# Performance work log

Measured on AMD Instinct MI355X. Metric: run time of the kernel, lower is better.

Reference implementation:

```python
import jax, jax.numpy as jnp
import numpy as np

BOS, PAD, EOS, UNK = 0, 1, 2, 3  # fairseq dictionary special-token ids
CHAR_VOCAB = 5000
DIM = 512
LATENT = 10000


def setup_inputs() -> dict:
    key = jax.random.key(0)
    k1, k2, k3 = jax.random.split(key, 3)
    # char-ngram ids per token: [B, T, max_char_len]
    x = jax.random.randint(k1, (8, 1024, 20), 0, CHAR_VOCAB, dtype=jnp.int64 if jax.config.jax_enable_x64 else jnp.int32)
    # char ngram embedding table (also serves as preset_emb for special tokens)
    char_table = jax.random.normal(k2, (CHAR_VOCAB, DIM), dtype=jnp.float32) * 0.05
    # fixed latent codebook, init std = latent**-0.5 as in the module
    latent_mat = jax.random.normal(k3, (LATENT, DIM), dtype=jnp.float32) * (LATENT ** -0.5)
    return {"x": x, "char_table": char_table, "latent_mat": latent_mat}


def reference(x, char_table, latent_mat):
    # --- CharacterNgramEmbedder: gather + sum-pool over char ngrams (pad masked) ---
    emb = char_table[x]                                   # [B, T, C, D]
    valid = (x != PAD)[..., None].astype(emb.dtype)       # pad ngrams contribute 0
    ngram_weight = jnp.sum(emb * valid, axis=2)           # [B, T, D]
    lang_emb = jnp.tanh(ngram_weight)

    # --- latent codebook attention: QK^T -> softmax -> V over fixed codebook ---
    latent_scores = jnp.einsum('btd,ld->btl', lang_emb, latent_mat)   # [B, T, L]
    latent_dist = jax.nn.softmax(latent_scores, axis=-1)
    latent_emb = jnp.einsum('btl,ld->btd', latent_dist, latent_mat)   # [B, T, D]
    sde_emb = lang_emb + latent_emb

    # --- preset_emb overwrite for special tokens (masked scatter) ---
    first = x[:, :, 0]                                    # [B, T]
    for tok in (PAD, BOS, EOS, UNK):
        sde_emb = jnp.where((first == tok)[..., None], char_table[tok], sde_emb)
    return sde_emb
```

## Files before the change

kernel.cpp:

```cpp
#include <hip/hip_runtime.h>

#define BT    8192
#define DIM   512
#define NLAT  10000
#define LPAD2 10240
#define NG    20
#define CV    5000

typedef short bf16x8 __attribute__((ext_vector_type(8)));
typedef float f32x4  __attribute__((ext_vector_type(4)));
typedef unsigned short u16;
typedef u16 u16x8 __attribute__((ext_vector_type(8)));
typedef u16 u16x4 __attribute__((ext_vector_type(4)));

static __device__ __forceinline__ u16 f2bf(float f) {
    union { float f; unsigned u; } v; v.f = f;
    unsigned r = v.u + 0x7FFF + ((v.u >> 16) & 1);
    return (u16)(r >> 16);
}
static __device__ __forceinline__ float bf2f(u16 b) {
    union { unsigned u; float f; } v; v.u = ((unsigned)b) << 16; return v.f;
}

static __device__ __forceinline__ void gload16(const void* g, void* l) {
    __builtin_amdgcn_global_load_lds(
        (const __attribute__((address_space(1))) unsigned int*)g,
        (__attribute__((address_space(3))) unsigned int*)l,
        16, 0, 0);
}

__global__ __launch_bounds__(256) void ct2bf_kernel(
        const float* __restrict__ ct, u16* __restrict__ ctb) {
    const long base = ((long)blockIdx.x * 256 + threadIdx.x) * 8;
    float4 a = *(const float4*)(ct + base);
    float4 b = *(const float4*)(ct + base + 4);
    u16x8 v = { f2bf(a.x), f2bf(a.y), f2bf(a.z), f2bf(a.w),
                f2bf(b.x), f2bf(b.y), f2bf(b.z), f2bf(b.w) };
    *(u16x8*)(ctb + base) = v;
}

__global__ __launch_bounds__(256) void lang_kernel(
        const int* __restrict__ x, const u16* __restrict__ ctb,
        float* __restrict__ lang, u16* __restrict__ qb) {
    const int wv  = threadIdx.x >> 6;
    const int tl  = threadIdx.x & 63;
    const int tok0 = blockIdx.x * 8 + wv * 2;
    const int* xr0 = x + tok0 * NG;
    const int* xr1 = xr0 + NG;
    float s0[8], s1[8];
    #pragma unroll
    for (int i = 0; i < 8; ++i) { s0[i] = 0.f; s1[i] = 0.f; }
    #pragma unroll
    for (int j = 0; j < NG; ++j) {
        int c0 = xr0[j], c1 = xr1[j];
        if (c0 != 1) {
            u16x8 v = *(const u16x8*)(ctb + (long)c0 * DIM + tl * 8);
            #pragma unroll
            for (int i = 0; i < 8; ++i) s0[i] += bf2f(v[i]);
        }
        if (c1 != 1) {
            u16x8 v = *(const u16x8*)(ctb + (long)c1 * DIM + tl * 8);
            #pragma unroll
            for (int i = 0; i < 8; ++i) s1[i] += bf2f(v[i]);
        }
    }
    #pragma unroll
    for (int p = 0; p < 2; ++p) {
        float* s = p ? s1 : s0;
        const long tok = tok0 + p;
        float4 lo, hi;
        lo.x = tanhf(s[0]); lo.y = tanhf(s[1]); lo.z = tanhf(s[2]); lo.w = tanhf(s[3]);
        hi.x = tanhf(s[4]); hi.y = tanhf(s[5]); hi.z = tanhf(s[6]); hi.w = tanhf(s[7]);
        *(float4*)(lang + tok * DIM + tl * 8)     = lo;
        *(float4*)(lang + tok * DIM + tl * 8 + 4) = hi;
        u16x8 o = { f2bf(lo.x), f2bf(lo.y), f2bf(lo.z), f2bf(lo.w),
                    f2bf(hi.x), f2bf(hi.y), f2bf(hi.z), f2bf(hi.w) };
        *(u16x8*)(qb + tok * DIM + tl * 8) = o;
    }
}

__global__ __launch_bounds__(256) void conv_kernel(
        const float* __restrict__ lm, u16* __restrict__ kvg, u16* __restrict__ latT) {
    __shared__ u16 tile[64][514];
    const int lb = blockIdx.x * 64;
    const int t  = threadIdx.x;

    #pragma unroll 4
    for (int i = 0; i < 16; ++i) {
        int ch  = t + i * 256;
        int r   = ch >> 6;
        int c8  = ch & 63;
        int row = lb + r;
        u16x8 v = {0,0,0,0,0,0,0,0};
        if (row < NLAT) {
            const float* src = lm + (long)row * DIM + c8 * 8;
            float4 a = *(const float4*)src;
            float4 b = *(const float4*)(src + 4);
            v[0]=f2bf(a.x); v[1]=f2bf(a.y); v[2]=f2bf(a.z); v[3]=f2bf(a.w);
            v[4]=f2bf(b.x); v[5]=f2bf(b.y); v[6]=f2bf(b.z); v[7]=f2bf(b.w);
        }
        *(u16x8*)(kvg + (long)row * DIM + c8 * 8) = v;
        #pragma unroll
        for (int j = 0; j < 8; ++j) tile[r][c8 * 8 + j] = v[j];
    }
    __syncthreads();
    #pragma unroll 4
    for (int i = 0; i < 16; ++i) {
        int ch = t + i * 256;
        int d  = ch >> 3;
        int c8 = ch & 7;
        u16x8 v;
        #pragma unroll
        for (int j = 0; j < 8; ++j) v[j] = tile[c8 * 8 + j][d];
        *(u16x8*)(latT + (long)d * LPAD2 + lb + c8 * 8) = v;
    }
}

#define G1_STAGE(buf, kt) {                                                    \
    const int k0_ = (kt) * 32;                                                 \
    {                                                                          \
        int ch_ = t;                                                           \
        int row_ = ch_ >> 2, c2_ = ch_ & 3;                                    \
        int sc_ = (c2_ ^ ((row_ >> 1) & 3)) * 8;                               \
        gload16(Q + (m0 + row_) * (long)DIM + k0_ + sc_, &lds[buf][ch_ * 8]);  \
        ch_ = t + 512; row_ = ch_ >> 2; c2_ = ch_ & 3;                         \
        sc_ = (c2_ ^ ((row_ >> 1) & 3)) * 8;                                   \
        gload16(Q + (m0 + row_) * (long)DIM + k0_ + sc_, &lds[buf][ch_ * 8]);  \
        row_ = t >> 2; c2_ = t & 3;                                            \
        sc_ = (c2_ ^ ((row_ >> 1) & 3)) * 8;                                   \
        gload16(Bgp + (long)row_ * DIM + k0_ + sc_, &lds[buf][8192 + t * 8]);  \
    }                                                                          \
}

#define G1_COMPUTE(buf) {                                                      \
    bf16x8 af_[4], bf_[4];                                                     \
    _Pragma("unroll")                                                          \
    for (int mf_ = 0; mf_ < 4; ++mf_) {                                        \
        const int rA_ = wm * 64 + mf_ * 16 + lr;                               \
        const int ck_ = g ^ ((rA_ >> 1) & 3);                                  \
        af_[mf_] = *(const bf16x8*)&lds[buf][rA_ * 32 + ck_ * 8];              \
    }                                                                          \
    _Pragma("unroll")                                                          \
    for (int nf_ = 0; nf_ < 4; ++nf_) {                                        \
        const int rB_ = wn * 64 + nf_ * 16 + lr;                               \
        const int ck_ = g ^ ((rB_ >> 1) & 3);                                  \
        bf_[nf_] = *(const bf16x8*)&lds[buf][8192 + rB_ * 32 + ck_ * 8];       \
    }                                                                          \
    __builtin_amdgcn_s_setprio(1);                                             \
    _Pragma("unroll")                                                          \
    for (int mf_ = 0; mf_ < 4; ++mf_)                                          \
        _Pragma("unroll")                                                      \
        for (int nf_ = 0; nf_ < 4; ++nf_)                                      \
            acc[mf_][nf_] = __builtin_amdgcn_mfma_f32_16x16x32_bf16(           \
                af_[mf_], bf_[nf_], acc[mf_][nf_], 0, 0, 0);                   \
    __builtin_amdgcn_s_setprio(0);                                             \
}

#define G1_STEP(kt, vmn) {                                                     \
    asm volatile("s_waitcnt vmcnt(" #vmn ")" ::: "memory");                    \
    __builtin_amdgcn_s_barrier();                                              \
    G1_COMPUTE((kt) % 3);                                                      \
    __builtin_amdgcn_s_barrier();                                              \
}

__global__ __launch_bounds__(512, 4) void gemm1_kernel(
        const u16* __restrict__ Q, const u16* __restrict__ L,
        u16* __restrict__ P, float* __restrict__ rowsum,
        int n0_global, int npanels, int pstride) {
    __shared__ u16 lds[3][12288];

    const int nwg = 32 * npanels;
    const int cpx = nwg >> 3;
    const int bid = blockIdx.x;
    const int wg  = (bid & 7) * cpx + (bid >> 3);
    int mb, nb;
    if (npanels == 80) {
        const int st = wg / 80, lt = wg % 80;
        const int lmb = lt & 7, lnb = lt >> 3;
        const int smb = st & 3, snb = st >> 2;
        mb = smb * 8 + lmb;
        nb = snb * 10 + lnb;
    } else {
        mb = wg & 31;
        nb = wg >> 5;
    }
    const long m0    = (long)mb * 256;
    const int  ncol0 = n0_global + nb * 128;

    const u16* Bgp = L + (long)ncol0 * DIM;

    const int t = threadIdx.x, lane = t & 63, w = t >> 6;
    const int wm = w >> 1, wn = w & 1;
    const int g = lane >> 4, lr = lane & 15;

    f32x4 acc[4][4];
    #pragma unroll
    for (int m = 0; m < 4; ++m)
        #pragma unroll
        for (int n = 0; n < 4; ++n) acc[m][n] = f32x4{0.f,0.f,0.f,0.f};

    G1_STAGE(0, 0);
    G1_STAGE(1, 1);
    G1_STAGE(2, 2);

    #pragma unroll 1
    for (int kt = 0; kt < 13; ++kt) {
        asm volatile("s_waitcnt vmcnt(6)" ::: "memory");
        __builtin_amdgcn_s_barrier();
        G1_COMPUTE(kt % 3);
        __builtin_amdgcn_s_barrier();
        G1_STAGE(kt % 3, kt + 3);
    }
    G1_STEP(13, 6);
    G1_STEP(14, 3);
    asm volatile("s_waitcnt vmcnt(0)" ::: "memory");
    __builtin_amdgcn_s_barrier();
    G1_COMPUTE(15 % 3);
    __syncthreads();

    u16* lds16 = &lds[0][0];
    #pragma unroll
    for (int mf = 0; mf < 4; ++mf)
        #pragma unroll
        for (int nf = 0; nf < 4; ++nf) {
            const int col = ncol0 + wn * 64 + nf * 16 + lr;
            const bool ok = (col < NLAT);
            const int lcol = wn * 64 + nf * 16 + lr;
            #pragma unroll
            for (int r = 0; r < 4; ++r) {
                float p = ok ? __expf(acc[mf][nf][r]) : 0.f;
                acc[mf][nf][r] = p;
                const int row = wm * 64 + mf * 16 + g * 4 + r;
                lds16[row * 128 + (lcol ^ ((row & 15) << 3))] = f2bf(p);
            }
        }

    #pragma unroll
    for (int mf = 0; mf < 4; ++mf) {
        float sv[4] = {0.f, 0.f, 0.f, 0.f};
        #pragma unroll
        for (int nf = 0; nf < 4; ++nf)
            #pragma unroll
            for (int r = 0; r < 4; ++r) sv[r] += acc[mf][nf][r];
        #pragma unroll
        for (int r = 0; r < 4; ++r) {
            float s = sv[r];
            s += __shfl_xor(s, 1); s += __shfl_xor(s, 2);
            s += __shfl_xor(s, 4); s += __shfl_xor(s, 8);
            if (lr == 0)
                atomicAdd(&rowsum[m0 + wm * 64 + mf * 16 + g * 4 + r], s);
        }
    }

    __syncthreads();
    const int pbase = ncol0 - n0_global;
    #pragma unroll
    for (int it = 0; it < 8; ++it) {
        const int flat = t + it * 512;
        const int row = flat >> 4, ck = flat & 15;
        u16x8 v = *(const u16x8*)&lds16[row * 128 + ((ck ^ (row & 15)) * 8)];
        *(u16x8*)(P + (m0 + row) * (long)pstride + pbase + ck * 8) = v;
    }
}

#define G_COMPUTE(buf) {                                                       \
    _Pragma("unroll")                                                          \
    for (int kc_ = 0; kc_ < 2; ++kc_) {                                        \
        const int xs_ = ((kc_ * 4 + g) ^ (lr & 7)) * 8;                        \
        bf16x8 af_[2], bf_[4];                                                 \
        _Pragma("unroll")                                                      \
        for (int mf_ = 0; mf_ < 2; ++mf_)                                      \
            af_[mf_] = *(const bf16x8*)&lds[buf][(wm * 32 + mf_ * 16 + lr) * 64 + xs_]; \
        _Pragma("unroll")                                                      \
        for (int nf_ = 0; nf_ < 4; ++nf_)                                      \
            bf_[nf_] = *(const bf16x8*)&lds[buf][8192 + (wn * 64 + nf_ * 16 + lr) * 64 + xs_]; \
        __builtin_amdgcn_s_setprio(1);                                         \
        _Pragma("unroll")                                                      \
        for (int mf_ = 0; mf_ < 2; ++mf_)                                      \
            _Pragma("unroll")                                                  \
            for (int nf_ = 0; nf_ < 4; ++nf_)                                  \
                acc[mf_][nf_] = __builtin_amdgcn_mfma_f32_16x16x32_bf16(       \
                    af_[mf_], bf_[nf_], acc[mf_][nf_], 0, 0, 0);               \
        __builtin_amdgcn_s_setprio(0);                                         \
    }                                                                          \
}

#define G2_STAGE(buf, kt) {                                                    \
    const int kloc_ = (step_off + (kt)) * 64;                                  \
    _Pragma("unroll")                                                          \
    for (int i_ = 0; i_ < 2; ++i_) {                                           \
        int ch_ = t + i_ * 512;                                                \
        int row_ = ch_ >> 3;                                                   \
        int sc_ = ((ch_ & 7) ^ (row_ & 7)) * 8;                                \
        gload16(P + (m0 + row_) * (long)pstride + kloc_ + sc_, &lds[buf][ch_ * 8]); \
        gload16(LT + (long)(nbase + row_) * LPAD2 + n0_global + kloc_ + sc_,   \
                &lds[buf][8192 + ch_ * 8]);                                    \
    }                                                                          \
}

__global__ __launch_bounds__(512, 4) void gemm2_kernel(
        const u16* __restrict__ P, const u16* __restrict__ LT,
        float* __restrict__ out, float* __restrict__ part0,
        int pstride, int kcols, int n0_global, int splitk, int accum) {
    __shared__ u16 lds[2][16384];

    const int nwg = 64 * 4 * splitk;
    const int cpx = nwg >> 3;
    const int bid = blockIdx.x;
    const int wg  = (bid & 7) * cpx + (bid >> 3);
    const int mb  = wg & 63;
    const int rest = wg >> 6;
    const int nb  = rest / splitk;
    const int s   = rest % splitk;

    const long m0    = (long)mb * 128;
    const int  nbase = nb * 128;

    const int nsteps = kcols / 64;
    const int q = nsteps / splitk, rr = nsteps % splitk;
    const int psteps   = q + (s < rr ? 1 : 0);
    const int step_off = s * q + (s < rr ? s : rr);

    const int t = threadIdx.x, lane = t & 63, w = t >> 6;
    const int wm = w >> 1, wn = w & 1;
    const int g = lane >> 4, lr = lane & 15;

    float* buf = (s == 0) ? out : part0;

    f32x4 acc[2][4];
    #pragma unroll
    for (int m = 0; m < 2; ++m)
        #pragma unroll
        for (int n = 0; n < 4; ++n) acc[m][n] = f32x4{0.f,0.f,0.f,0.f};

    G2_STAGE(0, 0);
    if (psteps > 1) G2_STAGE(1, 1);

    #pragma unroll 1
    for (int kt = 0; kt < psteps - 1; ++kt) {
        asm volatile("s_waitcnt vmcnt(4)" ::: "memory");
        __builtin_amdgcn_s_barrier();
        G_COMPUTE(kt & 1);
        __builtin_amdgcn_s_barrier();
        if (kt + 2 < psteps) G2_STAGE(kt & 1, kt + 2);
    }
    asm volatile("s_waitcnt vmcnt(0)" ::: "memory");
    __builtin_amdgcn_s_barrier();
    G_COMPUTE((psteps - 1) & 1);

    #pragma unroll
    for (int mf = 0; mf < 2; ++mf)
        #pragma unroll
        for (int nf = 0; nf < 4; ++nf) {
            const int col = nbase + wn * 64 + nf * 16 + lr;
            #pragma unroll
            for (int r = 0; r < 4; ++r) {
                const long row = m0 + wm * 32 + mf * 16 + g * 4 + r;
                float v = acc[mf][nf][r];
                if (accum) v += buf[row * DIM + col];
                buf[row * DIM + col] = v;
            }
        }
}

__global__ __launch_bounds__(256) void final_kernel(
        float* __restrict__ out, const float* __restrict__ part0,
        const float* __restrict__ lang, const float* __restrict__ rowsum,
        const int* __restrict__ x, const float* __restrict__ ct, int nparts) {
    const int tok   = blockIdx.x;
    const float inv = 1.f / rowsum[tok];
    const int first = x[tok * NG];
    #pragma unroll
    for (int i = 0; i < 2; ++i) {
        const int col = threadIdx.x + i * 256;
        float v = out[(long)tok * DIM + col];
        if (nparts > 1) v += part0[(long)tok * DIM + col];
        v = v * inv + lang[(long)tok * DIM + col];
        if (first < 4) v = ct[first * DIM + col];
        out[(long)tok * DIM + col] = v;
    }
}

extern "C" void kernel_launch(void* const* d_in, const int* in_sizes, int n_in,
                              void* d_out, int out_size, void* d_ws, size_t ws_size,
                              hipStream_t stream) {
    const int*   x  = (const int*)d_in[0];
    const float* ct = (const float*)d_in[1];
    const float* lm = (const float*)d_in[2];
    float* out = (float*)d_out;

    char* ws = (char*)d_ws;
    size_t off = 0;
    u16*   qb   = (u16*)(ws + off);   off += (size_t)BT * DIM * 2;
    float* lang = (float*)(ws + off); off += (size_t)BT * DIM * 4;
    u16*   kvg  = (u16*)(ws + off);   off += (size_t)LPAD2 * DIM * 2;
    u16*   latT = (u16*)(ws + off);   off += (size_t)DIM * LPAD2 * 2;
    u16*   ctb  = (u16*)(ws + off);   off += (size_t)CV * DIM * 2;
    float* rowsum = (float*)(ws + off); off += (size_t)BT * 4;
    u16*   P    = (u16*)(ws + off);
    const size_t fixed = off;

    const int panels_total = LPAD2 / 128;
    const size_t pfull = (size_t)BT * LPAD2 * 2;
    const size_t partb = (size_t)BT * DIM * 4;

    int splitk = 1, ppc = panels_total;
    float* part0 = out;
    if (ws_size >= fixed + pfull + partb) {
        splitk = 2;
        part0 = (float*)(ws + fixed + pfull);
    } else if (ws_size >= fixed + pfull) {
        splitk = 1;
    } else {
        size_t avail = (ws_size > fixed) ? (ws_size - fixed) : 0;
        size_t p = avail / ((size_t)BT * 128 * 2);
        ppc = (int)(p < 1 ? 1 : (p > (size_t)panels_total ? (size_t)panels_total : p));
        if (ppc & 1) ppc = (ppc > 1) ? ppc - 1 : 1;
    }
    const int pstride = ppc * 128;

    hipMemsetAsync(rowsum, 0, (size_t)BT * 4, stream);
    ct2bf_kernel<<<CV * DIM / (256 * 8), 256, 0, stream>>>(ct, ctb);
    lang_kernel<<<BT / 8, 256, 0, stream>>>(x, ctb, lang, qb);
    conv_kernel<<<LPAD2 / 64, 256, 0, stream>>>(lm, kvg, latT);

    int chunk = 0;
    for (int cs = 0; cs < panels_total; cs += ppc, ++chunk) {
        const int np = (panels_total - cs < ppc) ? (panels_total - cs) : ppc;
        gemm1_kernel<<<32 * np, 512, 0, stream>>>(qb, kvg, P, rowsum,
                                                  cs * 128, np, pstride);
        gemm2_kernel<<<64 * 4 * splitk, 512, 0, stream>>>(P, latT, out, part0,
                                                          pstride, np * 128, cs * 128,
                                                          splitk, chunk > 0 ? 1 : 0);
    }
    final_kernel<<<BT, 256, 0, stream>>>(out, part0, lang, rowsum, x, ct, splitk);
}
```

Baseline: 286.2 us.

## Retile gemm2 to 256x128 tiles with triple-buffered pipeline and split-K of four

The second GEMM (P @ latT) now uses the gemm1 tile shape: 256x128 output tiles, a K step of 32 and three LDS buffers in a deeper prefetch pipeline. This replaces 128x128 tiles with a K step of 64 and double buffering. Split-K rises from 2 to 4 when workspace allows, and the final kernel sums a variable number of partial buffers. The larger tiles raise data reuse per workgroup, and the higher split-K keeps enough workgroups to fill the GPU. The cost is more partial-sum traffic, more accumulator registers, and a fixed three-stage prologue that assumes each split has at least three K steps.

After: 272.7 us. -4.7%, faster.

```diff
diff --git a/kernel.cpp b/kernel.cpp
--- a/kernel.cpp
+++ b/kernel.cpp
@@ -114,22 +114,6 @@
         for (int j = 0; j < 8; ++j) v[j] = tile[c8 * 8 + j][d];
         *(u16x8*)(latT + (long)d * LPAD2 + lb + c8 * 8) = v;
     }
-}
-
-#define G1_STAGE(buf, kt) {                                                    \
-    const int k0_ = (kt) * 32;                                                 \
-    {                                                                          \
-        int ch_ = t;                                                           \
-        int row_ = ch_ >> 2, c2_ = ch_ & 3;                                    \
-        int sc_ = (c2_ ^ ((row_ >> 1) & 3)) * 8;                               \
-        gload16(Q + (m0 + row_) * (long)DIM + k0_ + sc_, &lds[buf][ch_ * 8]);  \
-        ch_ = t + 512; row_ = ch_ >> 2; c2_ = ch_ & 3;                         \
-        sc_ = (c2_ ^ ((row_ >> 1) & 3)) * 8;                                   \
-        gload16(Q + (m0 + row_) * (long)DIM + k0_ + sc_, &lds[buf][ch_ * 8]);  \
-        row_ = t >> 2; c2_ = t & 3;                                            \
-        sc_ = (c2_ ^ ((row_ >> 1) & 3)) * 8;                                   \
-        gload16(Bgp + (long)row_ * DIM + k0_ + sc_, &lds[buf][8192 + t * 8]);  \
-    }                                                                          \
 }
 
 #define G1_COMPUTE(buf) {                                                      \
@@ -156,6 +140,22 @@
     __builtin_amdgcn_s_setprio(0);                                             \
 }
 
+#define G1_STAGE(buf, kt) {                                                    \
+    const int k0_ = (kt) * 32;                                                 \
+    {                                                                          \
+        int ch_ = t;                                                           \
+        int row_ = ch_ >> 2, c2_ = ch_ & 3;                                    \
+        int sc_ = (c2_ ^ ((row_ >> 1) & 3)) * 8;                               \
+        gload16(Q + (m0 + row_) * (long)DIM + k0_ + sc_, &lds[buf][ch_ * 8]);  \
+        ch_ = t + 512; row_ = ch_ >> 2; c2_ = ch_ & 3;                         \
+        sc_ = (c2_ ^ ((row_ >> 1) & 3)) * 8;                                   \
+        gload16(Q + (m0 + row_) * (long)DIM + k0_ + sc_, &lds[buf][ch_ * 8]);  \
+        row_ = t >> 2; c2_ = t & 3;                                            \
+        sc_ = (c2_ ^ ((row_ >> 1) & 3)) * 8;                                   \
+        gload16(Bgp + (long)row_ * DIM + k0_ + sc_, &lds[buf][8192 + t * 8]);  \
+    }                                                                          \
+}
+
 #define G1_STEP(kt, vmn) {                                                     \
     asm volatile("s_waitcnt vmcnt(" #vmn ")" ::: "memory");                    \
     __builtin_amdgcn_s_barrier();                                              \
@@ -263,99 +263,95 @@
     }
 }
 
-#define G_COMPUTE(buf) {                                                       \
-    _Pragma("unroll")                                                          \
-    for (int kc_ = 0; kc_ < 2; ++kc_) {                                        \
-        const int xs_ = ((kc_ * 4 + g) ^ (lr & 7)) * 8;                        \
-        bf16x8 af_[2], bf_[4];                                                 \
-        _Pragma("unroll")                                                      \
-        for (int mf_ = 0; mf_ < 2; ++mf_)                                      \
-            af_[mf_] = *(const bf16x8*)&lds[buf][(wm * 32 + mf_ * 16 + lr) * 64 + xs_]; \
-        _Pragma("unroll")                                                      \
-        for (int nf_ = 0; nf_ < 4; ++nf_)                                      \
-            bf_[nf_] = *(const bf16x8*)&lds[buf][8192 + (wn * 64 + nf_ * 16 + lr) * 64 + xs_]; \
-        __builtin_amdgcn_s_setprio(1);                                         \
-        _Pragma("unroll")                                                      \
-        for (int mf_ = 0; mf_ < 2; ++mf_)                                      \
-            _Pragma("unroll")                                                  \
-            for (int nf_ = 0; nf_ < 4; ++nf_)                                  \
-                acc[mf_][nf_] = __builtin_amdgcn_mfma_f32_16x16x32_bf16(       \
-                    af_[mf_], bf_[nf_], acc[mf_][nf_], 0, 0, 0);               \
-        __builtin_amdgcn_s_setprio(0);                                         \
-    }                                                                          \
-}
-
 #define G2_STAGE(buf, kt) {                                                    \
-    const int kloc_ = (step_off + (kt)) * 64;                                  \
-    _Pragma("unroll")                                                          \
-    for (int i_ = 0; i_ < 2; ++i_) {                                           \
-        int ch_ = t + i_ * 512;                                                \
-        int row_ = ch_ >> 3;                                                   \
-        int sc_ = ((ch_ & 7) ^ (row_ & 7)) * 8;                                \
+    const int kloc_ = (step_off + (kt)) * 32;                                  \
+    {                                                                          \
+        int ch_ = t;                                                           \
+        int row_ = ch_ >> 2, c2_ = ch_ & 3;                                    \
+        int sc_ = (c2_ ^ ((row_ >> 1) & 3)) * 8;                               \
         gload16(P + (m0 + row_) * (long)pstride + kloc_ + sc_, &lds[buf][ch_ * 8]); \
+        ch_ = t + 512; row_ = ch_ >> 2; c2_ = ch_ & 3;                         \
+        sc_ = (c2_ ^ ((row_ >> 1) & 3)) * 8;                                   \
+        gload16(P + (m0 + row_) * (long)pstride + kloc_ + sc_, &lds[buf][ch_ * 8]); \
+        row_ = t >> 2; c2_ = t & 3;                                            \
+        sc_ = (c2_ ^ ((row_ >> 1) & 3)) * 8;                                   \
         gload16(LT + (long)(nbase + row_) * LPAD2 + n0_global + kloc_ + sc_,   \
-                &lds[buf][8192 + ch_ * 8]);                                    \
+                &lds[buf][8192 + t * 8]);                                      \
     }                                                                          \
 }
 
 __global__ __launch_bounds__(512, 4) void gemm2_kernel(
         const u16* __restrict__ P, const u16* __restrict__ LT,
-        float* __restrict__ out, float* __restrict__ part0,
+        float* __restrict__ out, float* __restrict__ parts,
         int pstride, int kcols, int n0_global, int splitk, int accum) {
-    __shared__ u16 lds[2][16384];
-
-    const int nwg = 64 * 4 * splitk;
+    __shared__ u16 lds[3][12288];
+
+    const int per = 4 * splitk;
+    const int nwg = 32 * per;
     const int cpx = nwg >> 3;
     const int bid = blockIdx.x;
     const int wg  = (bid & 7) * cpx + (bid >> 3);
-    const int mb  = wg & 63;
-    const int rest = wg >> 6;
-    const int nb  = rest / splitk;
-    const int s   = rest % splitk;
-
-    const long m0    = (long)mb * 128;
+    const int mb  = wg / per;
+    const int inr = wg % per;
+    const int nb  = inr / splitk;
+    const int s   = inr % splitk;
+
+    const long m0    = (long)mb * 256;
     const int  nbase = nb * 128;
 
-    const int nsteps = kcols / 64;
+    const int nsteps = kcols / 32;
     const int q = nsteps / splitk, rr = nsteps % splitk;
-    const int psteps   = q + (s < rr ? 1 : 0);
+    const int NT       = q + (s < rr ? 1 : 0);
     const int step_off = s * q + (s < rr ? s : rr);
 
     const int t = threadIdx.x, lane = t & 63, w = t >> 6;
     const int wm = w >> 1, wn = w & 1;
     const int g = lane >> 4, lr = lane & 15;
 
-    float* buf = (s == 0) ? out : part0;
-
-    f32x4 acc[2][4];
-    #pragma unroll
-    for (int m = 0; m < 2; ++m)
+    float* buf = (s == 0) ? out : (parts + (long)(s - 1) * BT * DIM);
+
+    f32x4 acc[4][4];
+    #pragma unroll
+    for (int m = 0; m < 4; ++m)
         #pragma unroll
         for (int n = 0; n < 4; ++n) acc[m][n] = f32x4{0.f,0.f,0.f,0.f};
 
     G2_STAGE(0, 0);
-    if (psteps > 1) G2_STAGE(1, 1);
+    G2_STAGE(1, 1);
+    G2_STAGE(2, 2);
 
     #pragma unroll 1
-    for (int kt = 0; kt < psteps - 1; ++kt) {
-        asm volatile("s_waitcnt vmcnt(4)" ::: "memory");
-        __builtin_amdgcn_s_barrier();
-        G_COMPUTE(kt & 1);
-        __builtin_amdgcn_s_barrier();
-        if (kt + 2 < psteps) G2_STAGE(kt & 1, kt + 2);
+    for (int kt = 0; kt < NT - 3; ++kt) {
+        asm volatile("s_waitcnt vmcnt(6)" ::: "memory");
+        __builtin_amdgcn_s_barrier();
+        G1_COMPUTE(kt % 3);
+        __builtin_amdgcn_s_barrier();
+        G2_STAGE(kt % 3, kt + 3);
+    }
+    {
+        asm volatile("s_waitcnt vmcnt(6)" ::: "memory");
+        __builtin_amdgcn_s_barrier();
+        G1_COMPUTE((NT - 3) % 3);
+        __builtin_amdgcn_s_barrier();
+    }
+    {
+        asm volatile("s_waitcnt vmcnt(3)" ::: "memory");
+        __builtin_amdgcn_s_barrier();
+        G1_COMPUTE((NT - 2) % 3);
+        __builtin_amdgcn_s_barrier();
     }
     asm volatile("s_waitcnt vmcnt(0)" ::: "memory");
     __builtin_amdgcn_s_barrier();
-    G_COMPUTE((psteps - 1) & 1);
-
-    #pragma unroll
-    for (int mf = 0; mf < 2; ++mf)
+    G1_COMPUTE((NT - 1) % 3);
+
+    #pragma unroll
+    for (int mf = 0; mf < 4; ++mf)
         #pragma unroll
         for (int nf = 0; nf < 4; ++nf) {
             const int col = nbase + wn * 64 + nf * 16 + lr;
             #pragma unroll
             for (int r = 0; r < 4; ++r) {
-                const long row = m0 + wm * 32 + mf * 16 + g * 4 + r;
+                const long row = m0 + wm * 64 + mf * 16 + g * 4 + r;
                 float v = acc[mf][nf][r];
                 if (accum) v += buf[row * DIM + col];
                 buf[row * DIM + col] = v;
@@ -364,7 +360,7 @@
 }
 
 __global__ __launch_bounds__(256) void final_kernel(
-        float* __restrict__ out, const float* __restrict__ part0,
+        float* __restrict__ out, const float* __restrict__ parts,
         const float* __restrict__ lang, const float* __restrict__ rowsum,
         const int* __restrict__ x, const float* __restrict__ ct, int nparts) {
     const int tok   = blockIdx.x;
@@ -373,11 +369,13 @@
     #pragma unroll
     for (int i = 0; i < 2; ++i) {
         const int col = threadIdx.x + i * 256;
-        float v = out[(long)tok * DIM + col];
-        if (nparts > 1) v += part0[(long)tok * DIM + col];
-        v = v * inv + lang[(long)tok * DIM + col];
+        const long idx = (long)tok * DIM + col;
+        float v = out[idx];
+        for (int p = 1; p < nparts; ++p)
+            v += parts[(long)(p - 1) * BT * DIM + idx];
+        v = v * inv + lang[idx];
         if (first < 4) v = ct[first * DIM + col];
-        out[(long)tok * DIM + col] = v;
+        out[idx] = v;
     }
 }
 
@@ -405,10 +403,13 @@
     const size_t partb = (size_t)BT * DIM * 4;
 
     int splitk = 1, ppc = panels_total;
-    float* part0 = out;
-    if (ws_size >= fixed + pfull + partb) {
+    float* parts = out;
+    if (ws_size >= fixed + pfull + 3 * partb) {
+        splitk = 4;
+        parts = (float*)(ws + fixed + pfull);
+    } else if (ws_size >= fixed + pfull + partb) {
         splitk = 2;
-        part0 = (float*)(ws + fixed + pfull);
+        parts = (float*)(ws + fixed + pfull);
     } else if (ws_size >= fixed + pfull) {
         splitk = 1;
     } else {
@@ -429,9 +430,9 @@
         const int np = (panels_total - cs < ppc) ? (panels_total - cs) : ppc;
         gemm1_kernel<<<32 * np, 512, 0, stream>>>(qb, kvg, P, rowsum,
                                                   cs * 128, np, pstride);
-        gemm2_kernel<<<64 * 4 * splitk, 512, 0, stream>>>(P, latT, out, part0,
+        gemm2_kernel<<<32 * 4 * splitk, 512, 0, stream>>>(P, latT, out, parts,
                                                           pstride, np * 128, cs * 128,
                                                           splitk, chunk > 0 ? 1 : 0);
     }
-    final_kernel<<<BT, 256, 0, stream>>>(out, part0, lang, rowsum, x, ct, splitk);
-}
+    final_kernel<<<BT, 256, 0, stream>>>(out, parts, lang, rowsum, x, ct, splitk);
+}
```
